# Optimization experiments

Measured on AMD Instinct MI355X. Metric: run time of the kernel, lower is better.

The kernel has to match this reference:

```python
import jax, jax.numpy as jnp
import numpy as np

HIDDEN = 1280
HEADS = 16
HEAD_DIM = HIDDEN // HEADS  # 80
INTER = 4608
DEPTH = 4
WIN = 64                     # tokens per attention window
FULL_BLOCKS = (3,)           # fullatt_block_indexes
EPS = 1e-6
SEQ = 3072


def setup_inputs() -> dict:
    key = jax.random.key(0)
    ks = jax.random.split(key, 20)
    sc = lambda *s: 0.02
    inp = {
        "x": jax.random.normal(ks[0], (SEQ, HIDDEN), jnp.float32),
        "rotary_pos_emb": jax.random.uniform(ks[1], (SEQ, HEAD_DIM // 2), jnp.float32) * 3.0,
        "s_aux": jax.random.normal(ks[2], (HEADS,), jnp.float32),
        "ln1_w": jnp.ones((DEPTH, HIDDEN), jnp.float32),
        "ln1_b": jnp.zeros((DEPTH, HIDDEN), jnp.float32),
        "qkv_w": jax.random.normal(ks[3], (DEPTH, HIDDEN, 3 * HIDDEN), jnp.float32) * 0.02,
        "qkv_b": jnp.zeros((DEPTH, 3 * HIDDEN), jnp.float32),
        "proj_w": jax.random.normal(ks[4], (DEPTH, HIDDEN, HIDDEN), jnp.float32) * 0.02,
        "proj_b": jnp.zeros((DEPTH, HIDDEN), jnp.float32),
        "ln2_w": jnp.ones((DEPTH, HIDDEN), jnp.float32),
        "ln2_b": jnp.zeros((DEPTH, HIDDEN), jnp.float32),
        "gate_w": jax.random.normal(ks[5], (DEPTH, HIDDEN, INTER), jnp.float32) * 0.02,
        "gate_b": jnp.zeros((DEPTH, INTER), jnp.float32),
        "up_w": jax.random.normal(ks[6], (DEPTH, HIDDEN, INTER), jnp.float32) * 0.02,
        "up_b": jnp.zeros((DEPTH, INTER), jnp.float32),
        "down_w": jax.random.normal(ks[7], (DEPTH, INTER, HIDDEN), jnp.float32) * 0.02,
        "down_b": jnp.zeros((DEPTH, HIDDEN), jnp.float32),
    }
    return inp


def _layer_norm(x, w, b):
    mu = jnp.mean(x, axis=-1, keepdims=True)
    var = jnp.mean(jnp.square(x - mu), axis=-1, keepdims=True)
    return (x - mu) * jax.lax.rsqrt(var + EPS) * w + b


def _rotate_half(x):
    x1, x2 = jnp.split(x, 2, axis=-1)
    return jnp.concatenate([-x2, x1], axis=-1)


def _apply_rotary(q, k, rot):
    # q,k: [S, H, D]; rot: [S, D/2]
    emb = jnp.concatenate([rot, rot], axis=-1)          # [S, D]
    cos = jnp.cos(emb)[:, None, :]
    sin = jnp.sin(emb)[:, None, :]
    q = q * cos + _rotate_half(q) * sin
    k = k * cos + _rotate_half(k) * sin
    return q, k


def _attention_with_sinks(q, k, v, s_aux):
    # q,k,v: [B, T, H, D]; block-diagonal within each of B windows.
    scale = 1.0 / jnp.sqrt(jnp.asarray(HEAD_DIM, q.dtype))
    scores = jnp.einsum("bqhd,bkhd->bhqk", q, k) * scale      # [B,H,q,k]
    sink = s_aux[None, :, None]                                # [1,H,1]
    m = jnp.maximum(jnp.max(scores, axis=-1), sink)            # [B,H,q]
    p = jnp.exp(scores - m[..., None])                         # [B,H,q,k]
    denom = jnp.sum(p, axis=-1) + jnp.exp(sink - m)            # [B,H,q]
    out = jnp.einsum("bhqk,bkhd->bqhd", p, v)
    out = out / jnp.transpose(denom, (0, 2, 1))[..., None]     # [B,q,H,D]
    return out


def reference(x, rotary_pos_emb, s_aux, ln1_w, ln1_b, qkv_w, qkv_b, proj_w, proj_b,
              ln2_w, ln2_b, gate_w, gate_b, up_w, up_b, down_w, down_b):
    S = x.shape[0]
    h = x
    for l in range(DEPTH):
        # --- attention ---
        hn = _layer_norm(h, ln1_w[l], ln1_b[l])
        qkv = hn @ qkv_w[l] + qkv_b[l]                          # [S, 3*HIDDEN]
        qkv = qkv.reshape(S, 3, HEADS, HEAD_DIM)
        q, k, v = qkv[:, 0], qkv[:, 1], qkv[:, 2]               # [S,H,D]
        q, k = _apply_rotary(q, k, rotary_pos_emb)
        if l in FULL_BLOCKS:
            B, T = 1, S                                         # full attention
        else:
            B, T = S // WIN, WIN                                # windowed (varlen block-diag)
        qw = q.reshape(B, T, HEADS, HEAD_DIM)
        kw = k.reshape(B, T, HEADS, HEAD_DIM)
        vw = v.reshape(B, T, HEADS, HEAD_DIM)
        o = _attention_with_sinks(qw, kw, vw, s_aux)            # [B,T,H,D]
        o = o.reshape(S, HIDDEN) @ proj_w[l] + proj_b[l]
        h = h + o
        # --- gated SiLU MLP ---
        hn = _layer_norm(h, ln2_w[l], ln2_b[l])
        g = jax.nn.silu(hn @ gate_w[l] + gate_b[l]) * (hn @ up_w[l] + up_b[l])
        h = h + g @ down_w[l] + down_b[l]
    return h
```

## Files before the change

kernel.cpp:

```cpp
#include <hip/hip_runtime.h>
#include <math.h>

typedef unsigned short u16;
typedef unsigned int u32;

using bf16x8 = __attribute__((ext_vector_type(8))) __bf16;
using f32x4  = __attribute__((ext_vector_type(4))) float;

#define SEQ 3072
#define HID 1280
#define NHEADS 16
#define HDIM 80
#define INTER 4608

#define LOG2E 1.44269504088896f
#define M2C   11.5415603f

__device__ __forceinline__ u16 f2bf(float f) {
    union { float f; u32 u; } v; v.f = f;
    u32 u = v.u;
    u32 r = u + 0x7fffu + ((u >> 16) & 1u);
    return (u16)(r >> 16);
}

__device__ __forceinline__ void gld16(const void* g, void* l) {
    __builtin_amdgcn_global_load_lds((const __attribute__((address_space(1))) void*)g,
                                     (__attribute__((address_space(3))) void*)l,
                                     16, 0, 0);
}

__device__ __forceinline__ bf16x8 frag8(const u16* base, int row, int ks, int quad) {
    int c = ks * 4 + quad;
    return *(const bf16x8*)&base[(row * 8 + (c ^ (row & 7))) * 8];
}

__global__ __launch_bounds__(256) void transpose_pack(const float* __restrict__ src,
                                                      u16* __restrict__ dst, int K, int N) {
    __shared__ float tile[32][33];
    int l = blockIdx.z;
    const float* s = src + (size_t)l * K * N;
    u16* d = dst + (size_t)l * N * K;
    int n0 = blockIdx.x * 32, k0 = blockIdx.y * 32;
    int tx = threadIdx.x & 31, ty = threadIdx.x >> 5;
#pragma unroll
    for (int i = 0; i < 4; i++) {
        int k = ty + i * 8;
        tile[k][tx] = s[(size_t)(k0 + k) * N + n0 + tx];
    }
    __syncthreads();
#pragma unroll
    for (int i = 0; i < 4; i++) {
        int n = ty + i * 8;
        d[(size_t)(n0 + n) * K + k0 + tx] = f2bf(tile[tx][n]);
    }
}

__global__ __launch_bounds__(256) void transpose_pack_gu(const float* __restrict__ src,
                                                         u16* __restrict__ dst, int K, int N,
                                                         int which) {
    __shared__ float tile[32][33];
    int l = blockIdx.z;
    const float* s = src + (size_t)l * K * N;
    u16* d = dst + (size_t)l * (2 * N) * K;
    int n0 = blockIdx.x * 32, k0 = blockIdx.y * 32;
    int tx = threadIdx.x & 31, ty = threadIdx.x >> 5;
#pragma unroll
    for (int i = 0; i < 4; i++) {
        int k = ty + i * 8;
        tile[k][tx] = s[(size_t)(k0 + k) * N + n0 + tx];
    }
    __syncthreads();
#pragma unroll
    for (int i = 0; i < 4; i++) {
        int n = ty + i * 8;
        int g = n0 + n;
        int n2 = ((g >> 4) << 5) | (g & 15) | (which << 4);
        d[(size_t)n2 * K + k0 + tx] = f2bf(tile[tx][n]);
    }
}

__global__ __launch_bounds__(256) void ln_kernel(const float* __restrict__ x,
                                                 const float* __restrict__ w,
                                                 const float* __restrict__ b,
                                                 u16* __restrict__ out) {
    int row = blockIdx.x;
    const float* xr = x + (size_t)row * HID;
    float v[5]; float s = 0.f, s2 = 0.f;
#pragma unroll
    for (int i = 0; i < 5; i++) { float t = xr[threadIdx.x + i * 256]; v[i] = t; s += t; s2 += t * t; }
#pragma unroll
    for (int off = 32; off > 0; off >>= 1) { s += __shfl_down(s, off); s2 += __shfl_down(s2, off); }
    __shared__ float red[8];
    int wv = threadIdx.x >> 6;
    if ((threadIdx.x & 63) == 0) { red[wv] = s; red[wv + 4] = s2; }
    __syncthreads();
    s  = red[0] + red[1] + red[2] + red[3];
    s2 = red[4] + red[5] + red[6] + red[7];
    float mu  = s * (1.f / HID);
    float var = s2 * (1.f / HID) - mu * mu;
    float rstd = rsqrtf(var + 1e-6f);
#pragma unroll
    for (int i = 0; i < 5; i++) {
        int col = threadIdx.x + i * 256;
        out[(size_t)row * HID + col] = f2bf((v[i] - mu) * rstd * w[col] + b[col]);
    }
}

__global__ __launch_bounds__(256) void qkv_pack(const float* __restrict__ qkv,
                                                const float* __restrict__ rot,
                                                u16* __restrict__ Qp, u16* __restrict__ Kp,
                                                u16* __restrict__ Vt) {
    const float QSC = 0.111803398874989485f * LOG2E;
    int s0 = blockIdx.x * 64, h = blockIdx.y;
    int tid = threadIdx.x;
    __shared__ u16 vlds[80 * 66];
    for (int idx = tid; idx < 64 * 40; idx += 256) {
        int r = idx / 40, d = idx - r * 40;
        const float* base = qkv + (size_t)(s0 + r) * 3840 + h * 80;
        float sn, cs;
        __sincosf(rot[(size_t)(s0 + r) * 40 + d], &sn, &cs);
        float q1 = base[d], q2 = base[d + 40];
        float k1 = base[1280 + d], k2 = base[1280 + d + 40];
        size_t ro = ((size_t)h * SEQ + s0 + r) * 128;
        Qp[ro + d]      = f2bf((q1 * cs - q2 * sn) * QSC);
        Qp[ro + d + 40] = f2bf((q2 * cs + q1 * sn) * QSC);
        Kp[ro + d]      = f2bf(k1 * cs - k2 * sn);
        Kp[ro + d + 40] = f2bf(k2 * cs + k1 * sn);
    }
    for (int idx = tid; idx < 64 * 48; idx += 256) {
        int r = idx / 48, d = 80 + (idx - r * 48);
        size_t ro = ((size_t)h * SEQ + s0 + r) * 128;
        Qp[ro + d] = 0; Kp[ro + d] = 0;
    }
    for (int idx = tid; idx < 64 * 80; idx += 256) {
        int r = idx / 80, d = idx - r * 80;
        vlds[d * 66 + r] = f2bf(qkv[(size_t)(s0 + r) * 3840 + 2560 + h * 80 + d]);
    }
    __syncthreads();
    for (int idx = tid; idx < 80 * 64; idx += 256) {
        int d = idx >> 6, ky = idx & 63;
        Vt[((size_t)h * 80 + d) * SEQ + s0 + ky] = vlds[d * 66 + ky];
    }
}

template<int MODE>
__global__ __launch_bounds__(256) void gemm_v3(const u16* __restrict__ A,
                                               const u16* __restrict__ B0,
                                               const u16* __restrict__ B1,
                                               const float* __restrict__ bias0,
                                               const float* __restrict__ bias1,
                                               const float* __restrict__ res,
                                               float* __restrict__ outf,
                                               u16* __restrict__ outh,
                                               int N, int K, int sx, int sy) {
    __shared__ u16 As[8192];
    __shared__ u16 Bs[(MODE == 1) ? 4096 : 8192];
    int tid = threadIdx.x, lane = tid & 63, wave = tid >> 6;
    int quad = lane >> 4, r15 = lane & 15;
    int f = blockIdx.x, xcd = f & 7, j = f >> 3;
    int bx, by;
    if (sx) { bx = xcd * sx + j % sx; by = j / sx; }
    else    { by = xcd * sy + j % sy; bx = j / sy; }
    int mBase = by * 128;
    int nBase = (MODE == 0) ? bx * 128 : bx * 64;

    int rs = tid >> 3, cs = tid & 7;
    int c0 = cs ^ (rs & 7);
    const u16* gA = A + (size_t)(mBase + rs) * K + c0 * 8;
    const u16* gB0 = B0 + (size_t)(nBase + rs) * K + c0 * 8;
    u16* dA = &As[(wave * 64) * 8];

    f32x4 acc[MODE == 0 ? 4 : 2][4] = {};

    int nK = K >> 6;
    for (int kt = 0; kt < nK; kt++) {
        const u16* a = gA + kt * 64;
        const u16* b0 = gB0 + kt * 64;
#pragma unroll
        for (int i = 0; i < 4; i++)
            gld16(a + (size_t)(i * 32) * K, dA + i * 2048);
#pragma unroll
        for (int i = 0; i < 2; i++)
            gld16(b0 + (size_t)(i * 32) * K, &Bs[(wave * 64) * 8 + i * 2048]);
        __syncthreads();

#pragma unroll
        for (int ks = 0; ks < 2; ks++) {
            bf16x8 af[2], bf[4];
#pragma unroll
            for (int mi = 0; mi < 2; mi++) af[mi] = frag8(As, wave * 32 + mi * 16 + r15, ks, quad);
#pragma unroll
            for (int ni = 0; ni < 4; ni++) bf[ni] = frag8(Bs, ni * 16 + r15, ks, quad);
#pragma unroll
            for (int mi = 0; mi < 2; mi++)
#pragma unroll
                for (int ni = 0; ni < 4; ni++)
                    acc[mi][ni] = __builtin_amdgcn_mfma_f32_16x16x32_bf16(af[mi], bf[ni], acc[mi][ni], 0, 0, 0);
        }
        __syncthreads();
    }

#pragma unroll
    for (int ni = 0; ni < 4; ni++) {
        int col = nBase + ni * 16 + r15;
        float bv = bias0[col];
#pragma unroll
        for (int mi = 0; mi < 2; mi++)
#pragma unroll
            for (int jj = 0; jj < 4; jj++) {
                int row = mBase + wave * 32 + mi * 16 + quad * 4 + jj;
                outf[(size_t)row * N + col] = acc[mi][ni][jj] + bv + res[(size_t)row * N + col];
            }
    }
}

template<int EPI>
__global__ __launch_bounds__(512, 2) void gemm8(const u16* __restrict__ A,
                                                const u16* __restrict__ B,
                                                const float* __restrict__ bias0,
                                                const float* __restrict__ bias1,
                                                float* __restrict__ outf,
                                                u16* __restrict__ outh,
                                                int N, int K) {
    __shared__ u16 sbuf[65536];
    int tid = threadIdx.x, lane = tid & 63, wave = tid >> 6;
    int quad = lane >> 4, r15 = lane & 15;
    int wm = wave >> 2, wn = wave & 3;

    int nwg = gridDim.x;
    int q8 = nwg >> 3, r8 = nwg & 7;
    int xcd = blockIdx.x & 7, j = blockIdx.x >> 3;
    int wg = (xcd < r8 ? xcd * (q8 + 1) : r8 * (q8 + 1) + (xcd - r8) * q8) + j;
    int bx = wg / 12, by = wg % 12;
    int mBase = by * 256, nBase = bx * 256;

    int rs = tid >> 3, cs = tid & 7;
    int c0 = cs ^ (rs & 7);
    const u16* gA = A + (size_t)(mBase + rs) * K + c0 * 8;
    const u16* gB = B + (size_t)(nBase + rs) * K + c0 * 8;
    int nK = K >> 6;

    f32x4 acc[8][4] = {};

    auto stage = [&](int bi, int kt, int p) {
        const u16* g = (p < 2) ? (gA + (size_t)kt * 64) : (gB + (size_t)kt * 64);
        int i0 = (p & 1) * 2;
        u16* d = &sbuf[bi * 32768 + ((p >= 2) ? 16384 : 0) + wave * 512 + i0 * 4096];
        gld16(g + (size_t)(i0 * 64) * K, d);
        gld16(g + (size_t)((i0 + 1) * 64) * K, d + 4096);
    };

#pragma unroll
    for (int p = 0; p < 4; p++) stage(0, 0, p);
    asm volatile("s_waitcnt vmcnt(0)" ::: "memory");
    __builtin_amdgcn_s_barrier();

    for (int kt = 0; kt < nK; kt++) {
        int cur = kt & 1;
        const u16* Ab = &sbuf[cur * 32768];
        const u16* Bb = &sbuf[cur * 32768 + 16384];
        bool pre = (kt + 1 < nK);
        bf16x8 bfr[4];
#pragma unroll
        for (int p = 0; p < 4; p++) {
            const int ks = p >> 1, mh = p & 1;
            bf16x8 af[4];
#pragma unroll
            for (int qi = 0; qi < 4; qi++)
                af[qi] = frag8(Ab, wm * 128 + mh * 64 + qi * 16 + r15, ks, quad);
            if ((p & 1) == 0) {
#pragma unroll
                for (int ni = 0; ni < 4; ni++)
                    bfr[ni] = frag8(Bb, wn * 64 + ni * 16 + r15, ks, quad);
            }
            if (pre) stage(cur ^ 1, kt + 1, p);
            __builtin_amdgcn_s_barrier();
            __builtin_amdgcn_s_setprio(1);
#pragma unroll
            for (int qi = 0; qi < 4; qi++)
#pragma unroll
                for (int ni = 0; ni < 4; ni++)
                    acc[mh * 4 + qi][ni] = __builtin_amdgcn_mfma_f32_16x16x32_bf16(
                        af[qi], bfr[ni], acc[mh * 4 + qi][ni], 0, 0, 0);
            __builtin_amdgcn_s_setprio(0);
            if (p < 3) __builtin_amdgcn_s_barrier();
        }
        if (pre) { asm volatile("s_waitcnt vmcnt(0)" ::: "memory"); }
        __builtin_amdgcn_s_barrier();
    }

    if constexpr (EPI == 0) {
#pragma unroll
        for (int ni = 0; ni < 4; ni++) {
            int col = nBase + wn * 64 + ni * 16 + r15;
            float bv = bias0[col];
#pragma unroll
            for (int mi = 0; mi < 8; mi++)
#pragma unroll
                for (int jj = 0; jj < 4; jj++) {
                    int row = mBase + wm * 128 + mi * 16 + quad * 4 + jj;
                    outf[(size_t)row * N + col] = acc[mi][ni][jj] + bv;
                }
        }
    } else {
#pragma unroll
        for (int pp = 0; pp < 2; pp++) {
            int col = (nBase >> 1) + wn * 32 + pp * 16 + r15;
            float gb = bias0[col], ub = bias1[col];
#pragma unroll
            for (int mi = 0; mi < 8; mi++)
#pragma unroll
                for (int jj = 0; jj < 4; jj++) {
                    int row = mBase + wm * 128 + mi * 16 + quad * 4 + jj;
                    float g = acc[mi][2 * pp][jj] + gb;
                    float u = acc[mi][2 * pp + 1][jj] + ub;
                    float sg = g / (1.f + __expf(-g));
                    outh[(size_t)row * INTER + col] = f2bf(sg * u);
                }
        }
    }
}

__global__ __launch_bounds__(256) void attn_kernel(const u16* __restrict__ Qp,
                                                   const u16* __restrict__ Kp,
                                                   const u16* __restrict__ Vt,
                                                   const float* __restrict__ s_aux,
                                                   u16* __restrict__ out, int windowed) {
    __shared__ u16 q_lds[8192];
    __shared__ u16 k_lds[8192];
    __shared__ u16 v_lds[5120];
    __shared__ u16 p_lds[64 * 72];

    int qt = blockIdx.x, h = blockIdx.y;
    int tid = threadIdx.x, lane = tid & 63, wave = tid >> 6;
    int quad = lane >> 4, r15 = lane & 15;

    const u16* Qh = Qp + (size_t)h * SEQ * 128;
    const u16* Kh = Kp + (size_t)h * SEQ * 128;
    const u16* Vh = Vt + (size_t)h * 80 * SEQ;

    {
        int q0 = qt * 64;
#pragma unroll
        for (int i = 0; i < 4; i++) {
            int slot = i * 256 + wave * 64 + lane;
            int row = slot >> 4, cc = slot & 15;
            int c = cc ^ (row & 7);
            gld16(Qh + (size_t)(q0 + row) * 128 + c * 8, &q_lds[(i * 256 + wave * 64) * 8]);
        }
    }
    __syncthreads();
    bf16x8 aq[3];
#pragma unroll
    for (int ks = 0; ks < 3; ks++) {
        int row = wave * 16 + r15;
        int c = ks * 4 + quad;
        aq[ks] = *(const bf16x8*)&q_lds[(row * 16 + (c ^ (row & 7))) * 8];
    }

    float l_j[4] = {0.f, 0.f, 0.f, 0.f};
    f32x4 ov[5] = {};

    int nT = windowed ? 1 : (SEQ / 64);
    int tBase = windowed ? qt : 0;
    for (int t = 0; t < nT; t++) {
        int key0 = (tBase + t) * 64;
        __syncthreads();
#pragma unroll
        for (int i = 0; i < 4; i++) {
            int slot = i * 256 + wave * 64 + lane;
            int row = slot >> 4, cc = slot & 15;
            int c = cc ^ (row & 7);
            gld16(Kh + (size_t)(key0 + row) * 128 + c * 8, &k_lds[(i * 256 + wave * 64) * 8]);
        }
#pragma unroll
        for (int i = 0; i < 2; i++) {
            int slot = i * 256 + wave * 64 + lane;
            int row = slot >> 3, cc = slot & 7;
            int c = cc ^ (row & 7);
            gld16(Vh + (size_t)row * SEQ + key0 + c * 8, &v_lds[(i * 256 + wave * 64) * 8]);
        }
        if (wave < 2) {
            int slot = 512 + wave * 64 + lane;
            int row = slot >> 3, cc = slot & 7;
            int c = cc ^ (row & 7);
            gld16(Vh + (size_t)row * SEQ + key0 + c * 8, &v_lds[(512 + wave * 64) * 8]);
        }
        __syncthreads();

        f32x4 sc[4];
#pragma unroll
        for (int nt = 0; nt < 4; nt++) {
            f32x4 z = {};
#pragma unroll
            for (int ks = 0; ks < 3; ks++) {
                int row = nt * 16 + r15;
                int c = ks * 4 + quad;
                bf16x8 bk = *(const bf16x8*)&k_lds[(row * 16 + (c ^ (row & 7))) * 8];
                z = __builtin_amdgcn_mfma_f32_16x16x32_bf16(aq[ks], bk, z, 0, 0, 0);
            }
            sc[nt] = z;
        }
#pragma unroll
        for (int nt = 0; nt < 4; nt++)
#pragma unroll
            for (int jj = 0; jj < 4; jj++) {
                float p = __builtin_amdgcn_exp2f(sc[nt][jj] - M2C);
                l_j[jj] += p;
                p_lds[(wave * 16 + quad * 4 + jj) * 72 + nt * 16 + r15] = f2bf(p);
            }
        asm volatile("s_waitcnt lgkmcnt(0)" ::: "memory");
        bf16x8 ap[2];
#pragma unroll
        for (int ks = 0; ks < 2; ks++)
            ap[ks] = *(const bf16x8*)&p_lds[(wave * 16 + r15) * 72 + ks * 32 + quad * 8];
#pragma unroll
        for (int t5 = 0; t5 < 5; t5++)
#pragma unroll
            for (int ks = 0; ks < 2; ks++) {
                int d = t5 * 16 + r15;
                int c = ks * 4 + quad;
                bf16x8 bv = *(const bf16x8*)&v_lds[(d * 8 + (c ^ (d & 7))) * 8];
                ov[t5] = __builtin_amdgcn_mfma_f32_16x16x32_bf16(ap[ks], bv, ov[t5], 0, 0, 0);
            }
    }
#pragma unroll
    for (int off = 1; off < 16; off <<= 1)
#pragma unroll
        for (int jj = 0; jj < 4; jj++)
            l_j[jj] += __shfl_xor(l_j[jj], off, 64);
    float sink = s_aux[h];
    float se = __builtin_amdgcn_exp2f(sink * LOG2E - M2C);
#pragma unroll
    for (int jj = 0; jj < 4; jj++) l_j[jj] = 1.f / (l_j[jj] + se);
#pragma unroll
    for (int t5 = 0; t5 < 5; t5++)
#pragma unroll
        for (int jj = 0; jj < 4; jj++) {
            int row = qt * 64 + wave * 16 + quad * 4 + jj;
            int d = t5 * 16 + r15;
            out[(size_t)row * HID + h * 80 + d] = f2bf(ov[t5][jj] * l_j[jj]);
        }
}

__global__ __launch_bounds__(256) void copy4_kernel(const float4* __restrict__ src,
                                                    float4* __restrict__ dst) {
    size_t i = (size_t)blockIdx.x * 256 + threadIdx.x;
    dst[i] = src[i];
}

extern "C" void kernel_launch(void* const* d_in, const int* in_sizes, int n_in,
                              void* d_out, int out_size, void* d_ws, size_t ws_size,
                              hipStream_t stream) {
    const float* x      = (const float*)d_in[0];
    const float* rot    = (const float*)d_in[1];
    const float* s_aux  = (const float*)d_in[2];
    const float* ln1_w  = (const float*)d_in[3];
    const float* ln1_b  = (const float*)d_in[4];
    const float* qkv_w  = (const float*)d_in[5];
    const float* qkv_b  = (const float*)d_in[6];
    const float* proj_w = (const float*)d_in[7];
    const float* proj_b = (const float*)d_in[8];
    const float* ln2_w  = (const float*)d_in[9];
    const float* ln2_b  = (const float*)d_in[10];
    const float* gate_w = (const float*)d_in[11];
    const float* gate_b = (const float*)d_in[12];
    const float* up_w   = (const float*)d_in[13];
    const float* up_b   = (const float*)d_in[14];
    const float* down_w = (const float*)d_in[15];
    const float* down_b = (const float*)d_in[16];

    char* ws = (char*)d_ws;
    size_t off = 0;
    auto alloc = [&](size_t n) -> char* {
        char* p = ws + off; off += (n + 255) & ~(size_t)255; return p;
    };
    u16* wt_qkv  = (u16*)alloc((size_t)4 * 3840 * 1280 * 2);
    u16* wt_proj = (u16*)alloc((size_t)4 * 1280 * 1280 * 2);
    u16* wt_gu   = (u16*)alloc((size_t)4 * 9216 * 1280 * 2);
    u16* wt_down = (u16*)alloc((size_t)4 * 1280 * 4608 * 2);
    float* h     = (float*)alloc((size_t)3072 * 1280 * 4);
    u16*  xn     = (u16*)alloc((size_t)3072 * 1280 * 2);
    float* gbuf  = (float*)alloc((size_t)3072 * 4608 * 4);
    float* qkvb  = gbuf;
    u16*  attnb  = (u16*)alloc((size_t)3072 * 1280 * 2);
    float* ubuf  = (float*)alloc((size_t)3072 * 4608 * 4);
    u16*  mbuf   = (u16*)alloc((size_t)3072 * 4608 * 2);
    u16* Qp  = (u16*)ubuf;
    u16* Kp  = Qp + (size_t)NHEADS * SEQ * 128;
    u16* Vtp = Kp + (size_t)NHEADS * SEQ * 128;

    transpose_pack<<<dim3(120, 40, 4), 256, 0, stream>>>(qkv_w,  wt_qkv,  1280, 3840);
    transpose_pack<<<dim3(40,  40, 4), 256, 0, stream>>>(proj_w, wt_proj, 1280, 1280);
    transpose_pack_gu<<<dim3(144, 40, 4), 256, 0, stream>>>(gate_w, wt_gu, 1280, 4608, 0);
    transpose_pack_gu<<<dim3(144, 40, 4), 256, 0, stream>>>(up_w,   wt_gu, 1280, 4608, 1);
    transpose_pack<<<dim3(40, 144, 4), 256, 0, stream>>>(down_w, wt_down, 4608, 1280);

    copy4_kernel<<<3840, 256, 0, stream>>>((const float4*)x, (float4*)h);

    for (int l = 0; l < 4; l++) {
        ln_kernel<<<3072, 256, 0, stream>>>(h, ln1_w + l * 1280, ln1_b + l * 1280, xn);
        gemm8<0><<<180, 512, 0, stream>>>(xn, wt_qkv + (size_t)l * 3840 * 1280,
                                          qkv_b + l * 3840, nullptr, qkvb, nullptr,
                                          3840, 1280);
        qkv_pack<<<dim3(48, 16), 256, 0, stream>>>(qkvb, rot, Qp, Kp, Vtp);
        attn_kernel<<<dim3(48, 16), 256, 0, stream>>>(Qp, Kp, Vtp, s_aux, attnb, (l == 3) ? 0 : 1);
        gemm_v3<1><<<480, 256, 0, stream>>>(attnb, wt_proj + (size_t)l * 1280 * 1280, nullptr,
                                            proj_b + l * 1280, nullptr, h, h, nullptr,
                                            1280, 1280, 0, 3);
        ln_kernel<<<3072, 256, 0, stream>>>(h, ln2_w + l * 1280, ln2_b + l * 1280, xn);
        gemm8<2><<<432, 512, 0, stream>>>(xn, wt_gu + (size_t)l * 9216 * 1280,
                                          gate_b + l * 4608, up_b + l * 4608,
                                          nullptr, mbuf, 9216, 1280);
        float* outp = (l == 3) ? (float*)d_out : h;
        gemm_v3<1><<<480, 256, 0, stream>>>(mbuf, wt_down + (size_t)l * 4608 * 1280, nullptr,
                                            down_b + l * 1280, nullptr, h, outp, nullptr,
                                            1280, 4608, 0, 3);
    }
}
```

Measured before the change: 1.651 ms.

## Unify GEMMs into triple-buffered templated gemm8 and widen full-attention query tile

The old gemm_v3 kernel is dropped and gemm8 is templated on the M tile. It now uses a 128-wide N tile and a three-stage shared-memory pipeline that prefetches two k-steps ahead with partial vmcnt waits. A residual-add epilogue lets the projection and down GEMMs use it too, and the QKV and gate/up grids double. The full-attention layer now runs a 128-row query tile per block so each K/V tile is reused across more queries. f2bf also switches to the native bf16 conversion. Together these aim at better load/compute overlap and more parallelism, at the cost of a smaller per-block output tile and more LDS per block.

```diff
diff --git a/kernel.cpp b/kernel.cpp
--- a/kernel.cpp
+++ b/kernel.cpp
@@ -17,10 +17,8 @@
 #define M2C   11.5415603f
 
 __device__ __forceinline__ u16 f2bf(float f) {
-    union { float f; u32 u; } v; v.f = f;
-    u32 u = v.u;
-    u32 r = u + 0x7fffu + ((u >> 16) & 1u);
-    return (u16)(r >> 16);
+    __bf16 h = (__bf16)f;
+    return __builtin_bit_cast(u16, h);
 }
 
 __device__ __forceinline__ void gld16(const void* g, void* l) {
@@ -143,86 +141,23 @@
     }
 }
 
-template<int MODE>
-__global__ __launch_bounds__(256) void gemm_v3(const u16* __restrict__ A,
-                                               const u16* __restrict__ B0,
-                                               const u16* __restrict__ B1,
-                                               const float* __restrict__ bias0,
-                                               const float* __restrict__ bias1,
-                                               const float* __restrict__ res,
-                                               float* __restrict__ outf,
-                                               u16* __restrict__ outh,
-                                               int N, int K, int sx, int sy) {
-    __shared__ u16 As[8192];
-    __shared__ u16 Bs[(MODE == 1) ? 4096 : 8192];
-    int tid = threadIdx.x, lane = tid & 63, wave = tid >> 6;
-    int quad = lane >> 4, r15 = lane & 15;
-    int f = blockIdx.x, xcd = f & 7, j = f >> 3;
-    int bx, by;
-    if (sx) { bx = xcd * sx + j % sx; by = j / sx; }
-    else    { by = xcd * sy + j % sy; bx = j / sy; }
-    int mBase = by * 128;
-    int nBase = (MODE == 0) ? bx * 128 : bx * 64;
-
-    int rs = tid >> 3, cs = tid & 7;
-    int c0 = cs ^ (rs & 7);
-    const u16* gA = A + (size_t)(mBase + rs) * K + c0 * 8;
-    const u16* gB0 = B0 + (size_t)(nBase + rs) * K + c0 * 8;
-    u16* dA = &As[(wave * 64) * 8];
-
-    f32x4 acc[MODE == 0 ? 4 : 2][4] = {};
-
-    int nK = K >> 6;
-    for (int kt = 0; kt < nK; kt++) {
-        const u16* a = gA + kt * 64;
-        const u16* b0 = gB0 + kt * 64;
-#pragma unroll
-        for (int i = 0; i < 4; i++)
-            gld16(a + (size_t)(i * 32) * K, dA + i * 2048);
-#pragma unroll
-        for (int i = 0; i < 2; i++)
-            gld16(b0 + (size_t)(i * 32) * K, &Bs[(wave * 64) * 8 + i * 2048]);
-        __syncthreads();
-
-#pragma unroll
-        for (int ks = 0; ks < 2; ks++) {
-            bf16x8 af[2], bf[4];
-#pragma unroll
-            for (int mi = 0; mi < 2; mi++) af[mi] = frag8(As, wave * 32 + mi * 16 + r15, ks, quad);
-#pragma unroll
-            for (int ni = 0; ni < 4; ni++) bf[ni] = frag8(Bs, ni * 16 + r15, ks, quad);
-#pragma unroll
-            for (int mi = 0; mi < 2; mi++)
-#pragma unroll
-                for (int ni = 0; ni < 4; ni++)
-                    acc[mi][ni] = __builtin_amdgcn_mfma_f32_16x16x32_bf16(af[mi], bf[ni], acc[mi][ni], 0, 0, 0);
-        }
-        __syncthreads();
-    }
-
-#pragma unroll
-    for (int ni = 0; ni < 4; ni++) {
-        int col = nBase + ni * 16 + r15;
-        float bv = bias0[col];
-#pragma unroll
-        for (int mi = 0; mi < 2; mi++)
-#pragma unroll
-            for (int jj = 0; jj < 4; jj++) {
-                int row = mBase + wave * 32 + mi * 16 + quad * 4 + jj;
-                outf[(size_t)row * N + col] = acc[mi][ni][jj] + bv + res[(size_t)row * N + col];
-            }
-    }
-}
-
-template<int EPI>
+template<int BM, int EPI>
 __global__ __launch_bounds__(512, 2) void gemm8(const u16* __restrict__ A,
                                                 const u16* __restrict__ B,
                                                 const float* __restrict__ bias0,
                                                 const float* __restrict__ bias1,
+                                                const float* __restrict__ res,
                                                 float* __restrict__ outf,
                                                 u16* __restrict__ outh,
                                                 int N, int K) {
-    __shared__ u16 sbuf[65536];
+    constexpr int MT   = 3072 / BM;
+    constexpr int MF   = BM / 32;
+    constexpr int LA   = BM / 64;
+    constexpr int LT   = LA + 2;
+    constexpr int ABUF = BM * 64;
+    constexpr int BUFU = ABUF + 8192;
+    __shared__ u16 sbuf[3 * BUFU];
+
     int tid = threadIdx.x, lane = tid & 63, wave = tid >> 6;
     int quad = lane >> 4, r15 = lane & 15;
     int wm = wave >> 2, wn = wave & 3;
@@ -231,8 +166,8 @@
     int q8 = nwg >> 3, r8 = nwg & 7;
     int xcd = blockIdx.x & 7, j = blockIdx.x >> 3;
     int wg = (xcd < r8 ? xcd * (q8 + 1) : r8 * (q8 + 1) + (xcd - r8) * q8) + j;
-    int bx = wg / 12, by = wg % 12;
-    int mBase = by * 256, nBase = bx * 256;
+    int bx = wg / MT, by = wg % MT;
+    int mBase = by * BM, nBase = bx * 128;
 
     int rs = tid >> 3, cs = tid & 7;
     int c0 = cs ^ (rs & 7);
@@ -240,96 +175,107 @@
     const u16* gB = B + (size_t)(nBase + rs) * K + c0 * 8;
     int nK = K >> 6;
 
-    f32x4 acc[8][4] = {};
-
-    auto stage = [&](int bi, int kt, int p) {
-        const u16* g = (p < 2) ? (gA + (size_t)kt * 64) : (gB + (size_t)kt * 64);
-        int i0 = (p & 1) * 2;
-        u16* d = &sbuf[bi * 32768 + ((p >= 2) ? 16384 : 0) + wave * 512 + i0 * 4096];
-        gld16(g + (size_t)(i0 * 64) * K, d);
-        gld16(g + (size_t)((i0 + 1) * 64) * K, d + 4096);
+    f32x4 acc[MF][2] = {};
+
+    auto stage1 = [&](int kt, int jl) {
+        int b = kt % 3;
+        if (jl < LA) {
+            gld16(gA + (size_t)kt * 64 + (size_t)(jl * 64) * K,
+                  &sbuf[b * BUFU + jl * 4096 + wave * 512]);
+        } else {
+            int i = jl - LA;
+            gld16(gB + (size_t)kt * 64 + (size_t)(i * 64) * K,
+                  &sbuf[b * BUFU + ABUF + i * 4096 + wave * 512]);
+        }
     };
 
 #pragma unroll
-    for (int p = 0; p < 4; p++) stage(0, 0, p);
-    asm volatile("s_waitcnt vmcnt(0)" ::: "memory");
+    for (int jl = 0; jl < LT; jl++) stage1(0, jl);
+#pragma unroll
+    for (int jl = 0; jl < LT; jl++) stage1(1, jl);
+    if constexpr (BM == 256) asm volatile("s_waitcnt vmcnt(6)" ::: "memory");
+    else                     asm volatile("s_waitcnt vmcnt(4)" ::: "memory");
     __builtin_amdgcn_s_barrier();
 
     for (int kt = 0; kt < nK; kt++) {
-        int cur = kt & 1;
-        const u16* Ab = &sbuf[cur * 32768];
-        const u16* Bb = &sbuf[cur * 32768 + 16384];
-        bool pre = (kt + 1 < nK);
-        bf16x8 bfr[4];
-#pragma unroll
-        for (int p = 0; p < 4; p++) {
-            const int ks = p >> 1, mh = p & 1;
-            bf16x8 af[4];
-#pragma unroll
-            for (int qi = 0; qi < 4; qi++)
-                af[qi] = frag8(Ab, wm * 128 + mh * 64 + qi * 16 + r15, ks, quad);
-            if ((p & 1) == 0) {
-#pragma unroll
-                for (int ni = 0; ni < 4; ni++)
-                    bfr[ni] = frag8(Bb, wn * 64 + ni * 16 + r15, ks, quad);
+        const u16* Ab = &sbuf[(kt % 3) * BUFU];
+        const u16* Bb = Ab + ABUF;
+        bool pre = (kt + 2 < nK);
+#pragma unroll
+        for (int ks = 0; ks < 2; ks++) {
+            bf16x8 af[MF], bf[2];
+#pragma unroll
+            for (int mi = 0; mi < MF; mi++)
+                af[mi] = frag8(Ab, wm * (BM / 2) + mi * 16 + r15, ks, quad);
+#pragma unroll
+            for (int ni = 0; ni < 2; ni++)
+                bf[ni] = frag8(Bb, wn * 32 + ni * 16 + r15, ks, quad);
+            if (pre) {
+#pragma unroll
+                for (int jl = 0; jl < LT / 2; jl++) stage1(kt + 2, ks * (LT / 2) + jl);
             }
-            if (pre) stage(cur ^ 1, kt + 1, p);
             __builtin_amdgcn_s_barrier();
             __builtin_amdgcn_s_setprio(1);
 #pragma unroll
-            for (int qi = 0; qi < 4; qi++)
-#pragma unroll
-                for (int ni = 0; ni < 4; ni++)
-                    acc[mh * 4 + qi][ni] = __builtin_amdgcn_mfma_f32_16x16x32_bf16(
-                        af[qi], bfr[ni], acc[mh * 4 + qi][ni], 0, 0, 0);
+            for (int mi = 0; mi < MF; mi++)
+#pragma unroll
+                for (int ni = 0; ni < 2; ni++)
+                    acc[mi][ni] = __builtin_amdgcn_mfma_f32_16x16x32_bf16(
+                        af[mi], bf[ni], acc[mi][ni], 0, 0, 0);
             __builtin_amdgcn_s_setprio(0);
-            if (p < 3) __builtin_amdgcn_s_barrier();
-        }
-        if (pre) { asm volatile("s_waitcnt vmcnt(0)" ::: "memory"); }
+            if (ks == 0) __builtin_amdgcn_s_barrier();
+        }
+        if (pre) {
+            if constexpr (BM == 256) asm volatile("s_waitcnt vmcnt(6)" ::: "memory");
+            else                     asm volatile("s_waitcnt vmcnt(4)" ::: "memory");
+        } else if (kt + 1 < nK) {
+            asm volatile("s_waitcnt vmcnt(0)" ::: "memory");
+        }
         __builtin_amdgcn_s_barrier();
     }
 
-    if constexpr (EPI == 0) {
-#pragma unroll
-        for (int ni = 0; ni < 4; ni++) {
-            int col = nBase + wn * 64 + ni * 16 + r15;
+    if constexpr (EPI == 2) {
+        int col = (nBase >> 1) + wn * 16 + r15;
+        float gb = bias0[col], ub = bias1[col];
+#pragma unroll
+        for (int mi = 0; mi < MF; mi++)
+#pragma unroll
+            for (int jj = 0; jj < 4; jj++) {
+                int row = mBase + wm * (BM / 2) + mi * 16 + quad * 4 + jj;
+                float g = acc[mi][0][jj] + gb;
+                float u = acc[mi][1][jj] + ub;
+                float sg = g / (1.f + __expf(-g));
+                outh[(size_t)row * INTER + col] = f2bf(sg * u);
+            }
+    } else {
+#pragma unroll
+        for (int ni = 0; ni < 2; ni++) {
+            int col = nBase + wn * 32 + ni * 16 + r15;
             float bv = bias0[col];
 #pragma unroll
-            for (int mi = 0; mi < 8; mi++)
+            for (int mi = 0; mi < MF; mi++)
 #pragma unroll
                 for (int jj = 0; jj < 4; jj++) {
-                    int row = mBase + wm * 128 + mi * 16 + quad * 4 + jj;
-                    outf[(size_t)row * N + col] = acc[mi][ni][jj] + bv;
+                    int row = mBase + wm * (BM / 2) + mi * 16 + quad * 4 + jj;
+                    float v = acc[mi][ni][jj] + bv;
+                    if constexpr (EPI == 1) v += res[(size_t)row * N + col];
+                    outf[(size_t)row * N + col] = v;
                 }
         }
-    } else {
-#pragma unroll
-        for (int pp = 0; pp < 2; pp++) {
-            int col = (nBase >> 1) + wn * 32 + pp * 16 + r15;
-            float gb = bias0[col], ub = bias1[col];
-#pragma unroll
-            for (int mi = 0; mi < 8; mi++)
-#pragma unroll
-                for (int jj = 0; jj < 4; jj++) {
-                    int row = mBase + wm * 128 + mi * 16 + quad * 4 + jj;
-                    float g = acc[mi][2 * pp][jj] + gb;
-                    float u = acc[mi][2 * pp + 1][jj] + ub;
-                    float sg = g / (1.f + __expf(-g));
-                    outh[(size_t)row * INTER + col] = f2bf(sg * u);
-                }
-        }
-    }
-}
-
+    }
+}
+
+template<int QR>
 __global__ __launch_bounds__(256) void attn_kernel(const u16* __restrict__ Qp,
                                                    const u16* __restrict__ Kp,
                                                    const u16* __restrict__ Vt,
                                                    const float* __restrict__ s_aux,
-                                                   u16* __restrict__ out, int windowed) {
-    __shared__ u16 q_lds[8192];
+                                                   u16* __restrict__ out) {
+    constexpr int MH = QR / 64;
+    __shared__ u16 q_lds[QR * 128];
     __shared__ u16 k_lds[8192];
     __shared__ u16 v_lds[5120];
-    __shared__ u16 p_lds[64 * 72];
+    __shared__ u16 p_lds[QR * 72];
 
     int qt = blockIdx.x, h = blockIdx.y;
     int tid = threadIdx.x, lane = tid & 63, wave = tid >> 6;
@@ -340,29 +286,31 @@
     const u16* Vh = Vt + (size_t)h * 80 * SEQ;
 
     {
-        int q0 = qt * 64;
-#pragma unroll
-        for (int i = 0; i < 4; i++) {
-            int slot = i * 256 + wave * 64 + lane;
+        int q0 = qt * QR;
+#pragma unroll
+        for (int i = 0; i < QR / 16; i++) {
+            int slot = i * 256 + tid;
             int row = slot >> 4, cc = slot & 15;
             int c = cc ^ (row & 7);
             gld16(Qh + (size_t)(q0 + row) * 128 + c * 8, &q_lds[(i * 256 + wave * 64) * 8]);
         }
     }
     __syncthreads();
-    bf16x8 aq[3];
-#pragma unroll
-    for (int ks = 0; ks < 3; ks++) {
-        int row = wave * 16 + r15;
-        int c = ks * 4 + quad;
-        aq[ks] = *(const bf16x8*)&q_lds[(row * 16 + (c ^ (row & 7))) * 8];
-    }
-
-    float l_j[4] = {0.f, 0.f, 0.f, 0.f};
-    f32x4 ov[5] = {};
-
-    int nT = windowed ? 1 : (SEQ / 64);
-    int tBase = windowed ? qt : 0;
+    bf16x8 aq[MH][3];
+#pragma unroll
+    for (int mh = 0; mh < MH; mh++)
+#pragma unroll
+        for (int ks = 0; ks < 3; ks++) {
+            int row = wave * (16 * MH) + mh * 16 + r15;
+            int c = ks * 4 + quad;
+            aq[mh][ks] = *(const bf16x8*)&q_lds[(row * 16 + (c ^ (row & 7))) * 8];
+        }
+
+    float l_j[MH][4] = {};
+    f32x4 ov[MH][5] = {};
+
+    int nT = (QR == 64) ? 1 : (SEQ / 64);
+    int tBase = (QR == 64) ? qt : 0;
     for (int t = 0; t < nT; t++) {
         int key0 = (tBase + t) * 64;
         __syncthreads();
@@ -388,32 +336,35 @@
         }
         __syncthreads();
 
-        f32x4 sc[4];
-#pragma unroll
-        for (int nt = 0; nt < 4; nt++) {
-            f32x4 z = {};
+        f32x4 sc[MH][4] = {};
+#pragma unroll
+        for (int nt = 0; nt < 4; nt++)
 #pragma unroll
             for (int ks = 0; ks < 3; ks++) {
                 int row = nt * 16 + r15;
                 int c = ks * 4 + quad;
                 bf16x8 bk = *(const bf16x8*)&k_lds[(row * 16 + (c ^ (row & 7))) * 8];
-                z = __builtin_amdgcn_mfma_f32_16x16x32_bf16(aq[ks], bk, z, 0, 0, 0);
+#pragma unroll
+                for (int mh = 0; mh < MH; mh++)
+                    sc[mh][nt] = __builtin_amdgcn_mfma_f32_16x16x32_bf16(aq[mh][ks], bk, sc[mh][nt], 0, 0, 0);
             }
-            sc[nt] = z;
-        }
-#pragma unroll
-        for (int nt = 0; nt < 4; nt++)
-#pragma unroll
-            for (int jj = 0; jj < 4; jj++) {
-                float p = __builtin_amdgcn_exp2f(sc[nt][jj] - M2C);
-                l_j[jj] += p;
-                p_lds[(wave * 16 + quad * 4 + jj) * 72 + nt * 16 + r15] = f2bf(p);
-            }
+#pragma unroll
+        for (int mh = 0; mh < MH; mh++)
+#pragma unroll
+            for (int nt = 0; nt < 4; nt++)
+#pragma unroll
+                for (int jj = 0; jj < 4; jj++) {
+                    float p = __builtin_amdgcn_exp2f(sc[mh][nt][jj] - M2C);
+                    l_j[mh][jj] += p;
+                    p_lds[(wave * 16 * MH + mh * 16 + quad * 4 + jj) * 72 + nt * 16 + r15] = f2bf(p);
+                }
         asm volatile("s_waitcnt lgkmcnt(0)" ::: "memory");
-        bf16x8 ap[2];
-#pragma unroll
-        for (int ks = 0; ks < 2; ks++)
-            ap[ks] = *(const bf16x8*)&p_lds[(wave * 16 + r15) * 72 + ks * 32 + quad * 8];
+        bf16x8 ap[MH][2];
+#pragma unroll
+        for (int mh = 0; mh < MH; mh++)
+#pragma unroll
+            for (int ks = 0; ks < 2; ks++)
+                ap[mh][ks] = *(const bf16x8*)&p_lds[(wave * 16 * MH + mh * 16 + r15) * 72 + ks * 32 + quad * 8];
 #pragma unroll
         for (int t5 = 0; t5 < 5; t5++)
 #pragma unroll
@@ -421,26 +372,34 @@
                 int d = t5 * 16 + r15;
                 int c = ks * 4 + quad;
                 bf16x8 bv = *(const bf16x8*)&v_lds[(d * 8 + (c ^ (d & 7))) * 8];
-                ov[t5] = __builtin_amdgcn_mfma_f32_16x16x32_bf16(ap[ks], bv, ov[t5], 0, 0, 0);
+#pragma unroll
+                for (int mh = 0; mh < MH; mh++)
+                    ov[mh][t5] = __builtin_amdgcn_mfma_f32_16x16x32_bf16(ap[mh][ks], bv, ov[mh][t5], 0, 0, 0);
             }
     }
 #pragma unroll
-    for (int off = 1; off < 16; off <<= 1)
-#pragma unroll
-        for (int jj = 0; jj < 4; jj++)
-            l_j[jj] += __shfl_xor(l_j[jj], off, 64);
+    for (int mh = 0; mh < MH; mh++)
+#pragma unroll
+        for (int off = 1; off < 16; off <<= 1)
+#pragma unroll
+            for (int jj = 0; jj < 4; jj++)
+                l_j[mh][jj] += __shfl_xor(l_j[mh][jj], off, 64);
     float sink = s_aux[h];
     float se = __builtin_amdgcn_exp2f(sink * LOG2E - M2C);
 #pragma unroll
-    for (int jj = 0; jj < 4; jj++) l_j[jj] = 1.f / (l_j[jj] + se);
-#pragma unroll
-    for (int t5 = 0; t5 < 5; t5++)
-#pragma unroll
-        for (int jj = 0; jj < 4; jj++) {
-            int row = qt * 64 + wave * 16 + quad * 4 + jj;
-            int d = t5 * 16 + r15;
-            out[(size_t)row * HID + h * 80 + d] = f2bf(ov[t5][jj] * l_j[jj]);
-        }
+    for (int mh = 0; mh < MH; mh++)
+#pragma unroll
+        for (int jj = 0; jj < 4; jj++) l_j[mh][jj] = 1.f / (l_j[mh][jj] + se);
+#pragma unroll
+    for (int mh = 0; mh < MH; mh++)
+#pragma unroll
+        for (int t5 = 0; t5 < 5; t5++)
+#pragma unroll
+            for (int jj = 0; jj < 4; jj++) {
+                int row = qt * QR + wave * 16 * MH + mh * 16 + quad * 4 + jj;
+                int d = t5 * 16 + r15;
+                out[(size_t)row * HID + h * 80 + d] = f2bf(ov[mh][t5][jj] * l_j[mh][jj]);
+            }
 }
 
 __global__ __launch_bounds__(256) void copy4_kernel(const float4* __restrict__ src,
@@ -500,21 +459,24 @@
 
     for (int l = 0; l < 4; l++) {
         ln_kernel<<<3072, 256, 0, stream>>>(h, ln1_w + l * 1280, ln1_b + l * 1280, xn);
-        gemm8<0><<<180, 512, 0, stream>>>(xn, wt_qkv + (size_t)l * 3840 * 1280,
-                                          qkv_b + l * 3840, nullptr, qkvb, nullptr,
-                                          3840, 1280);
+        gemm8<256, 0><<<360, 512, 0, stream>>>(xn, wt_qkv + (size_t)l * 3840 * 1280,
+                                               qkv_b + l * 3840, nullptr, nullptr,
+                                               qkvb, nullptr, 3840, 1280);
         qkv_pack<<<dim3(48, 16), 256, 0, stream>>>(qkvb, rot, Qp, Kp, Vtp);
-        attn_kernel<<<dim3(48, 16), 256, 0, stream>>>(Qp, Kp, Vtp, s_aux, attnb, (l == 3) ? 0 : 1);
-        gemm_v3<1><<<480, 256, 0, stream>>>(attnb, wt_proj + (size_t)l * 1280 * 1280, nullptr,
-                                            proj_b + l * 1280, nullptr, h, h, nullptr,
-                                            1280, 1280, 0, 3);
+        if (l == 3)
+            attn_kernel<128><<<dim3(SEQ / 128, 16), 256, 0, stream>>>(Qp, Kp, Vtp, s_aux, attnb);
+        else
+            attn_kernel<64><<<dim3(SEQ / 64, 16), 256, 0, stream>>>(Qp, Kp, Vtp, s_aux, attnb);
+        gemm8<128, 1><<<240, 512, 0, stream>>>(attnb, wt_proj + (size_t)l * 1280 * 1280,
+                                               proj_b + l * 1280, nullptr, h,
+                                               h, nullptr, 1280, 1280);
         ln_kernel<<<3072, 256, 0, stream>>>(h, ln2_w + l * 1280, ln2_b + l * 1280, xn);
-        gemm8<2><<<432, 512, 0, stream>>>(xn, wt_gu + (size_t)l * 9216 * 1280,
-                                          gate_b + l * 4608, up_b + l * 4608,
-                                          nullptr, mbuf, 9216, 1280);
+        gemm8<256, 2><<<864, 512, 0, stream>>>(xn, wt_gu + (size_t)l * 9216 * 1280,
+                                               gate_b + l * 4608, up_b + l * 4608, nullptr,
+                                               nullptr, mbuf, 9216, 1280);
         float* outp = (l == 3) ? (float*)d_out : h;
-        gemm_v3<1><<<480, 256, 0, stream>>>(mbuf, wt_down + (size_t)l * 4608 * 1280, nullptr,
-                                            down_b + l * 1280, nullptr, h, outp, nullptr,
-                                            1280, 4608, 0, 3);
-    }
-}
+        gemm8<128, 1><<<240, 512, 0, stream>>>(mbuf, wt_down + (size_t)l * 4608 * 1280,
+                                               down_b + l * 1280, nullptr, h,
+                                               outp, nullptr, 1280, 4608);
+    }
+}
```

After: 1.557 ms. 1.06x faster.
